# Kernel tuning notes

Measured on AMD Instinct MI355X. Metric: run time of the kernel, lower is better.

The kernel has to match this reference:

```python
import jax, jax.numpy as jnp
import numpy as np

K, S, P = 3, 2, 2  # kernel_size, stride, padding (dilation=1)


def _unfold(xp, k, s, oh, ow):
    """Extract k*k strided patches from a padded array.

    xp: (..., Hp, Wp) -> (..., k*k, oh, ow), window-position ordering (kh, kw)
    matching torch.nn.Unfold (channel-major handled by caller).
    """
    return jnp.stack(
        [xp[..., i:i + s * (oh - 1) + 1:s, j:j + s * (ow - 1) + 1:s]
         for i in range(K) for j in range(K)],
        axis=-3,
    )


def setup_inputs() -> dict:
    key = jax.random.key(0)
    x = jax.random.normal(key, (8, 256, 128, 128), dtype=jnp.float32)
    return {"x": x}


def reference(x):
    b, c, h, w = x.shape
    oh = (h - K + 2 * P) // S + 1
    ow = (w - K + 2 * P) // S + 1

    # channel-wise L2 norm, computed BEFORE unfolding (padding contributes 0 either way)
    n = jnp.sqrt(jnp.sum(x * x, axis=1))            # (b, h, w)
    n_pad = jnp.pad(n, ((0, 0), (P, P), (P, P)))
    n_patch = _unfold(n_pad, K, S, oh, ow)          # (b, k*k, oh, ow)
    # weighting_fn = softmax over the k*k window positions (torch dim=1 of unfolded norm)
    wts = jax.nn.softmax(n_patch, axis=1)           # (b, k*k, oh, ow)

    x_pad = jnp.pad(x, ((0, 0), (0, 0), (P, P), (P, P)))
    x_patch = _unfold(x_pad, K, S, oh, ow)          # (b, c, k*k, oh, ow)

    # weighted sum over window positions
    return jnp.sum(wts[:, None] * x_patch, axis=2)  # (b, c, oh, ow)
```

## Files before the change

### kernel.cpp

```cpp
#include <hip/hip_runtime.h>
#include <math.h>

#define BATCH 8
#define CH    256
#define H     128
#define W     128
#define HW    (H * W)
#define OH    65
#define OW    65
#define NPIX  (OH * OW)
#define TPB   512
#define WAVES 8
#define CPW   (CH / WAVES)

__global__ __launch_bounds__(TPB, 6) void fused_kernel(const float* __restrict__ x,
                                                       float* __restrict__ out) {
    const int b    = blockIdx.x & 7;
    const int oh   = blockIdx.x >> 3;
    const int tid  = threadIdx.x;
    const int lane = tid & 63;
    const int wv   = tid >> 6;

    int  rowc[3];
    bool rv[3];
    #pragma unroll
    for (int r = 0; r < 3; ++r) {
        int ih = oh * 2 + r - 2;
        rv[r]   = (unsigned)ih < (unsigned)H;
        rowc[r] = ih < 0 ? 0 : (ih > H - 1 ? H - 1 : ih);
    }

    __shared__ float part[WAVES][3][W];
    __shared__ float nrm[3][W];
    __shared__ float wls[OH][9];

    const float2* xw2 = (const float2*)x + (size_t)(b * CH + wv * CPW) * (HW / 2);
    const int base0 = rowc[0] * (W / 2) + lane;
    const int base1 = rowc[1] * (W / 2) + lane;
    const int base2 = rowc[2] * (W / 2) + lane;

    float2 a0 = {0.f, 0.f}, a1 = {0.f, 0.f}, a2 = {0.f, 0.f};
    #pragma unroll 8
    for (int c = 0; c < CPW; ++c) {
        const size_t cb = (size_t)c * (HW / 2);
        float2 v0 = xw2[cb + base0];
        float2 v1 = xw2[cb + base1];
        float2 v2 = xw2[cb + base2];
        a0.x += v0.x * v0.x; a0.y += v0.y * v0.y;
        a1.x += v1.x * v1.x; a1.y += v1.y * v1.y;
        a2.x += v2.x * v2.x; a2.y += v2.y * v2.y;
    }
    *(float2*)&part[wv][0][2 * lane] = a0;
    *(float2*)&part[wv][1][2 * lane] = a1;
    *(float2*)&part[wv][2][2 * lane] = a2;
    __syncthreads();

    if (tid < 3 * W) {
        int r = tid >> 7, col = tid & (W - 1);
        float s = 0.f;
        #pragma unroll
        for (int w = 0; w < WAVES; ++w) s += part[w][r][col];
        nrm[r][col] = sqrtf(s);
    }
    __syncthreads();

    if (tid < OH) {
        const int ow  = tid;
        const int iw0 = ow * 2 - 2;
        float nv[9];
        bool  val[9];
        float m = 0.0f;
        #pragma unroll
        for (int kh = 0; kh < 3; ++kh) {
            bool vh = rv[kh];
            #pragma unroll
            for (int kw = 0; kw < 3; ++kw) {
                int iw = iw0 + kw;
                int k  = kh * 3 + kw;
                bool v = vh && ((unsigned)iw < (unsigned)W);
                val[k] = v;
                nv[k]  = v ? nrm[kh][iw] : 0.0f;
                m = fmaxf(m, nv[k]);
            }
        }
        float denom = 0.0f, wt[9];
        #pragma unroll
        for (int k = 0; k < 9; ++k) {
            float e = __expf(nv[k] - m);
            denom += e;
            wt[k] = val[k] ? e : 0.0f;
        }
        float inv = 1.0f / denom;
        #pragma unroll
        for (int k = 0; k < 9; ++k) wls[ow][k] = wt[k] * inv;
    }
    __syncthreads();

    const float wA0 = wls[lane][2], wA1 = wls[lane][5], wA2 = wls[lane][8];
    const float wB0 = wls[lane + 1][0], wC0 = wls[lane + 1][1];
    const float wB1 = wls[lane + 1][3], wC1 = wls[lane + 1][4];
    const float wB2 = wls[lane + 1][6], wC2 = wls[lane + 1][7];

    float* ob = out + (size_t)(b * CH + wv * CPW) * NPIX + (size_t)oh * OW;
    #pragma unroll 4
    for (int c = 0; c < CPW; ++c) {
        const size_t cb = (size_t)c * (HW / 2);
        float2 v0 = xw2[cb + base0];
        float2 v1 = xw2[cb + base1];
        float2 v2 = xw2[cb + base2];
        float S = wB0 * v0.x + wC0 * v0.y
                + wB1 * v1.x + wC1 * v1.y
                + wB2 * v2.x + wC2 * v2.y;
        float T = wA0 * v0.x + wA1 * v1.x + wA2 * v2.x;
        float Sp = __shfl_up(S, 1);
        float res = (lane == 0) ? T : T + Sp;
        ob[(size_t)c * NPIX + lane] = res;
        if (lane == 63) ob[(size_t)c * NPIX + 64] = S;
    }
}

extern "C" void kernel_launch(void* const* d_in, const int* in_sizes, int n_in,
                              void* d_out, int out_size, void* d_ws, size_t ws_size,
                              hipStream_t stream) {
    const float* x = (const float*)d_in[0];
    float* out = (float*)d_out;
    (void)d_ws; (void)ws_size;
    fused_kernel<<<BATCH * OH, TPB, 0, stream>>>(x, out);
}
```

Baseline: 232.2 us.

## Split norm into separate pass and compute two output rows per block

The fused kernel is split in two. A norm kernel streams x once and writes per-pixel channel L2 norms to the workspace. The pool kernel then reads those norms and processes two output rows per block, loading 5 input rows instead of 3 per row, so the overlapping input row is reused within the block. This removes the redundant norm pass over x in every block. In exchange it adds a second launch and a workspace round trip, and the pool kernel has fewer blocks.

```diff
diff --git a/kernel.cpp b/kernel.cpp
--- a/kernel.cpp
+++ b/kernel.cpp
@@ -9,113 +9,141 @@
 #define OH    65
 #define OW    65
 #define NPIX  (OH * OW)
-#define TPB   512
-#define WAVES 8
-#define CPW   (CH / WAVES)
 
-__global__ __launch_bounds__(TPB, 6) void fused_kernel(const float* __restrict__ x,
-                                                       float* __restrict__ out) {
+__global__ __launch_bounds__(256) void norm_kernel(const float4* __restrict__ x4,
+                                                   float* __restrict__ nrm) {
+    const int b    = blockIdx.x >> 6;
+    const int t    = blockIdx.x & 63;
+    const int lane = threadIdx.x & 63;
+    const int wv   = threadIdx.x >> 6;
+
+    const float4* p = x4 + (size_t)(b * CH + wv * 64) * (HW / 4) + t * 64 + lane;
+    float4 a = {0.f, 0.f, 0.f, 0.f};
+    #pragma unroll 8
+    for (int c = 0; c < 64; ++c) {
+        float4 v = p[(size_t)c * (HW / 4)];
+        a.x += v.x * v.x; a.y += v.y * v.y;
+        a.z += v.z * v.z; a.w += v.w * v.w;
+    }
+    __shared__ float part[4][256];
+    ((float4*)part[wv])[lane] = a;
+    __syncthreads();
+    float s = part[0][threadIdx.x] + part[1][threadIdx.x]
+            + part[2][threadIdx.x] + part[3][threadIdx.x];
+    nrm[(size_t)b * HW + t * 256 + threadIdx.x] = sqrtf(s);
+}
+
+#define OHT   33
+#define K2TPB 512
+#define CPW   32
+
+__global__ __launch_bounds__(K2TPB) void pool_kernel(const float* __restrict__ x,
+                                                     const float* __restrict__ nrm,
+                                                     float* __restrict__ out) {
     const int b    = blockIdx.x & 7;
-    const int oh   = blockIdx.x >> 3;
+    const int ohT  = blockIdx.x >> 3;
+    const int oh0  = ohT * 2;
+    const bool hasB = (oh0 + 1) < OH;
     const int tid  = threadIdx.x;
     const int lane = tid & 63;
     const int wv   = tid >> 6;
 
-    int  rowc[3];
-    bool rv[3];
+    int rowc[5];
     #pragma unroll
-    for (int r = 0; r < 3; ++r) {
-        int ih = oh * 2 + r - 2;
-        rv[r]   = (unsigned)ih < (unsigned)H;
+    for (int r = 0; r < 5; ++r) {
+        int ih = oh0 * 2 - 2 + r;
         rowc[r] = ih < 0 ? 0 : (ih > H - 1 ? H - 1 : ih);
     }
 
-    __shared__ float part[WAVES][3][W];
-    __shared__ float nrm[3][W];
-    __shared__ float wls[OH][9];
+    __shared__ float ns[5][W];
+    __shared__ float wls[2 * OH][9];
+
+    for (int id = tid; id < 5 * W; id += K2TPB) {
+        int r = id >> 7, col = id & (W - 1);
+        ns[r][col] = nrm[(size_t)b * HW + rowc[r] * W + col];
+    }
+    __syncthreads();
+
+    if (tid < 2 * OH) {
+        int ohl = tid >= OH ? 1 : 0;
+        int ow  = tid - ohl * OH;
+        int oh  = oh0 + ohl;
+        if (oh < OH) {
+            int iw0 = ow * 2 - 2;
+            float nv[9]; bool val[9]; float m = 0.0f;
+            #pragma unroll
+            for (int kh = 0; kh < 3; ++kh) {
+                int ih = oh * 2 + kh - 2;
+                bool vh = (unsigned)ih < (unsigned)H;
+                int rL = 2 * ohl + kh;
+                #pragma unroll
+                for (int kw = 0; kw < 3; ++kw) {
+                    int iw = iw0 + kw;
+                    int k  = kh * 3 + kw;
+                    bool v = vh && ((unsigned)iw < (unsigned)W);
+                    val[k] = v;
+                    nv[k]  = v ? ns[rL][iw] : 0.0f;
+                    m = fmaxf(m, nv[k]);
+                }
+            }
+            float denom = 0.0f, wt[9];
+            #pragma unroll
+            for (int k = 0; k < 9; ++k) {
+                float e = __expf(nv[k] - m);
+                denom += e;
+                wt[k] = val[k] ? e : 0.0f;
+            }
+            float inv = 1.0f / denom;
+            #pragma unroll
+            for (int k = 0; k < 9; ++k) wls[tid][k] = wt[k] * inv;
+        }
+    }
+    __syncthreads();
+
+    const float aA0 = wls[lane][2],     aA1 = wls[lane][5],     aA2 = wls[lane][8];
+    const float aB0 = wls[lane + 1][0], aC0 = wls[lane + 1][1];
+    const float aB1 = wls[lane + 1][3], aC1 = wls[lane + 1][4];
+    const float aB2 = wls[lane + 1][6], aC2 = wls[lane + 1][7];
+    const float bA0 = wls[OH + lane][2],     bA1 = wls[OH + lane][5],     bA2 = wls[OH + lane][8];
+    const float bB0 = wls[OH + lane + 1][0], bC0 = wls[OH + lane + 1][1];
+    const float bB1 = wls[OH + lane + 1][3], bC1 = wls[OH + lane + 1][4];
+    const float bB2 = wls[OH + lane + 1][6], bC2 = wls[OH + lane + 1][7];
 
     const float2* xw2 = (const float2*)x + (size_t)(b * CH + wv * CPW) * (HW / 2);
     const int base0 = rowc[0] * (W / 2) + lane;
     const int base1 = rowc[1] * (W / 2) + lane;
     const int base2 = rowc[2] * (W / 2) + lane;
+    const int base3 = rowc[3] * (W / 2) + lane;
+    const int base4 = rowc[4] * (W / 2) + lane;
 
-    float2 a0 = {0.f, 0.f}, a1 = {0.f, 0.f}, a2 = {0.f, 0.f};
-    #pragma unroll 8
-    for (int c = 0; c < CPW; ++c) {
-        const size_t cb = (size_t)c * (HW / 2);
-        float2 v0 = xw2[cb + base0];
-        float2 v1 = xw2[cb + base1];
-        float2 v2 = xw2[cb + base2];
-        a0.x += v0.x * v0.x; a0.y += v0.y * v0.y;
-        a1.x += v1.x * v1.x; a1.y += v1.y * v1.y;
-        a2.x += v2.x * v2.x; a2.y += v2.y * v2.y;
-    }
-    *(float2*)&part[wv][0][2 * lane] = a0;
-    *(float2*)&part[wv][1][2 * lane] = a1;
-    *(float2*)&part[wv][2][2 * lane] = a2;
-    __syncthreads();
-
-    if (tid < 3 * W) {
-        int r = tid >> 7, col = tid & (W - 1);
-        float s = 0.f;
-        #pragma unroll
-        for (int w = 0; w < WAVES; ++w) s += part[w][r][col];
-        nrm[r][col] = sqrtf(s);
-    }
-    __syncthreads();
-
-    if (tid < OH) {
-        const int ow  = tid;
-        const int iw0 = ow * 2 - 2;
-        float nv[9];
-        bool  val[9];
-        float m = 0.0f;
-        #pragma unroll
-        for (int kh = 0; kh < 3; ++kh) {
-            bool vh = rv[kh];
-            #pragma unroll
-            for (int kw = 0; kw < 3; ++kw) {
-                int iw = iw0 + kw;
-                int k  = kh * 3 + kw;
-                bool v = vh && ((unsigned)iw < (unsigned)W);
-                val[k] = v;
-                nv[k]  = v ? nrm[kh][iw] : 0.0f;
-                m = fmaxf(m, nv[k]);
-            }
-        }
-        float denom = 0.0f, wt[9];
-        #pragma unroll
-        for (int k = 0; k < 9; ++k) {
-            float e = __expf(nv[k] - m);
-            denom += e;
-            wt[k] = val[k] ? e : 0.0f;
-        }
-        float inv = 1.0f / denom;
-        #pragma unroll
-        for (int k = 0; k < 9; ++k) wls[ow][k] = wt[k] * inv;
-    }
-    __syncthreads();
-
-    const float wA0 = wls[lane][2], wA1 = wls[lane][5], wA2 = wls[lane][8];
-    const float wB0 = wls[lane + 1][0], wC0 = wls[lane + 1][1];
-    const float wB1 = wls[lane + 1][3], wC1 = wls[lane + 1][4];
-    const float wB2 = wls[lane + 1][6], wC2 = wls[lane + 1][7];
-
-    float* ob = out + (size_t)(b * CH + wv * CPW) * NPIX + (size_t)oh * OW;
+    float* ob = out + (size_t)(b * CH + wv * CPW) * NPIX + (size_t)oh0 * OW;
     #pragma unroll 4
     for (int c = 0; c < CPW; ++c) {
         const size_t cb = (size_t)c * (HW / 2);
         float2 v0 = xw2[cb + base0];
         float2 v1 = xw2[cb + base1];
         float2 v2 = xw2[cb + base2];
-        float S = wB0 * v0.x + wC0 * v0.y
-                + wB1 * v1.x + wC1 * v1.y
-                + wB2 * v2.x + wC2 * v2.y;
-        float T = wA0 * v0.x + wA1 * v1.x + wA2 * v2.x;
-        float Sp = __shfl_up(S, 1);
-        float res = (lane == 0) ? T : T + Sp;
-        ob[(size_t)c * NPIX + lane] = res;
-        if (lane == 63) ob[(size_t)c * NPIX + 64] = S;
+        float SA = aB0 * v0.x + aC0 * v0.y
+                 + aB1 * v1.x + aC1 * v1.y
+                 + aB2 * v2.x + aC2 * v2.y;
+        float TA = aA0 * v0.x + aA1 * v1.x + aA2 * v2.x;
+        float SpA = __shfl_up(SA, 1);
+        float resA = (lane == 0) ? TA : TA + SpA;
+        float* oc = ob + (size_t)c * NPIX;
+        oc[lane] = resA;
+        if (lane == 63) oc[64] = SA;
+        if (hasB) {
+            float2 v3 = xw2[cb + base3];
+            float2 v4 = xw2[cb + base4];
+            float SB = bB0 * v2.x + bC0 * v2.y
+                     + bB1 * v3.x + bC1 * v3.y
+                     + bB2 * v4.x + bC2 * v4.y;
+            float TB = bA0 * v2.x + bA1 * v3.x + bA2 * v4.x;
+            float SpB = __shfl_up(SB, 1);
+            float resB = (lane == 0) ? TB : TB + SpB;
+            oc[OW + lane] = resB;
+            if (lane == 63) oc[OW + 64] = SB;
+        }
     }
 }
 
@@ -123,7 +151,9 @@
                               void* d_out, int out_size, void* d_ws, size_t ws_size,
                               hipStream_t stream) {
     const float* x = (const float*)d_in[0];
-    float* out = (float*)d_out;
-    (void)d_ws; (void)ws_size;
-    fused_kernel<<<BATCH * OH, TPB, 0, stream>>>(x, out);
+    float* out  = (float*)d_out;
+    float* nbuf = (float*)d_ws;
+
+    norm_kernel<<<512, 256, 0, stream>>>((const float4*)x, nbuf);
+    pool_kernel<<<BATCH * OHT, K2TPB, 0, stream>>>(x, nbuf, out);
 }
```

New measurement: 224.1 us. -3.5%, faster.

## Split channel-norm into separate kernel and split pooling across channel groups

Applied to the files above, without the earlier changes.

Computes the per-pixel channel L2 norm in a dedicated kernel that reads each input element once and stores norms in workspace. The pooling kernel then loads precomputed norms instead of recomputing them from overlapping rows, and splits channels into two groups to double the grid size. This cuts the redundant input reads caused by overlapping windows. In exchange it adds a second launch and a small workspace round-trip.

```diff
diff --git a/kernel.cpp b/kernel.cpp
--- a/kernel.cpp
+++ b/kernel.cpp
@@ -9,77 +9,76 @@
 #define OH    65
 #define OW    65
 #define NPIX  (OH * OW)
-#define TPB   512
-#define WAVES 8
-#define CPW   (CH / WAVES)
 
-__global__ __launch_bounds__(TPB, 6) void fused_kernel(const float* __restrict__ x,
-                                                       float* __restrict__ out) {
-    const int b    = blockIdx.x & 7;
-    const int oh   = blockIdx.x >> 3;
+__global__ __launch_bounds__(256) void norm_kernel(const float4* __restrict__ x4,
+                                                   float* __restrict__ nrm) {
+    const int b    = blockIdx.x >> 6;
+    const int t    = blockIdx.x & 63;
+    const int lane = threadIdx.x & 63;
+    const int wv   = threadIdx.x >> 6;
+
+    const float4* p = x4 + (size_t)(b * CH + wv * 64) * (HW / 4) + t * 64 + lane;
+    float4 a = {0.f, 0.f, 0.f, 0.f};
+    #pragma unroll 8
+    for (int c = 0; c < 64; ++c) {
+        float4 v = p[(size_t)c * (HW / 4)];
+        a.x += v.x * v.x; a.y += v.y * v.y;
+        a.z += v.z * v.z; a.w += v.w * v.w;
+    }
+    __shared__ float part[4][256];
+    ((float4*)part[wv])[lane] = a;
+    __syncthreads();
+    float s = part[0][threadIdx.x] + part[1][threadIdx.x]
+            + part[2][threadIdx.x] + part[3][threadIdx.x];
+    nrm[(size_t)b * HW + t * 256 + threadIdx.x] = sqrtf(s);
+}
+
+#define K2TPB 256
+#define CPW   32
+#define CGC   128
+
+__global__ __launch_bounds__(K2TPB) void pool_kernel(const float* __restrict__ x,
+                                                     const float* __restrict__ nrm,
+                                                     float* __restrict__ out) {
+    const int b   = blockIdx.x & 7;
+    const int rem = blockIdx.x >> 3;
+    const int oh  = rem % OH;
+    const int cg  = rem / OH;
     const int tid  = threadIdx.x;
     const int lane = tid & 63;
     const int wv   = tid >> 6;
 
     int  rowc[3];
-    bool rv[3];
     #pragma unroll
     for (int r = 0; r < 3; ++r) {
         int ih = oh * 2 + r - 2;
-        rv[r]   = (unsigned)ih < (unsigned)H;
         rowc[r] = ih < 0 ? 0 : (ih > H - 1 ? H - 1 : ih);
     }
 
-    __shared__ float part[WAVES][3][W];
-    __shared__ float nrm[3][W];
+    __shared__ float ns[3][W];
     __shared__ float wls[OH][9];
 
-    const float2* xw2 = (const float2*)x + (size_t)(b * CH + wv * CPW) * (HW / 2);
-    const int base0 = rowc[0] * (W / 2) + lane;
-    const int base1 = rowc[1] * (W / 2) + lane;
-    const int base2 = rowc[2] * (W / 2) + lane;
-
-    float2 a0 = {0.f, 0.f}, a1 = {0.f, 0.f}, a2 = {0.f, 0.f};
-    #pragma unroll 8
-    for (int c = 0; c < CPW; ++c) {
-        const size_t cb = (size_t)c * (HW / 2);
-        float2 v0 = xw2[cb + base0];
-        float2 v1 = xw2[cb + base1];
-        float2 v2 = xw2[cb + base2];
-        a0.x += v0.x * v0.x; a0.y += v0.y * v0.y;
-        a1.x += v1.x * v1.x; a1.y += v1.y * v1.y;
-        a2.x += v2.x * v2.x; a2.y += v2.y * v2.y;
-    }
-    *(float2*)&part[wv][0][2 * lane] = a0;
-    *(float2*)&part[wv][1][2 * lane] = a1;
-    *(float2*)&part[wv][2][2 * lane] = a2;
-    __syncthreads();
-
-    if (tid < 3 * W) {
-        int r = tid >> 7, col = tid & (W - 1);
-        float s = 0.f;
-        #pragma unroll
-        for (int w = 0; w < WAVES; ++w) s += part[w][r][col];
-        nrm[r][col] = sqrtf(s);
+    for (int id = tid; id < 3 * W; id += K2TPB) {
+        int r = id >> 7, col = id & (W - 1);
+        ns[r][col] = nrm[(size_t)b * HW + rowc[r] * W + col];
     }
     __syncthreads();
 
     if (tid < OH) {
         const int ow  = tid;
         const int iw0 = ow * 2 - 2;
-        float nv[9];
-        bool  val[9];
-        float m = 0.0f;
+        float nv[9]; bool val[9]; float m = 0.0f;
         #pragma unroll
         for (int kh = 0; kh < 3; ++kh) {
-            bool vh = rv[kh];
+            int ih = oh * 2 + kh - 2;
+            bool vh = (unsigned)ih < (unsigned)H;
             #pragma unroll
             for (int kw = 0; kw < 3; ++kw) {
                 int iw = iw0 + kw;
                 int k  = kh * 3 + kw;
                 bool v = vh && ((unsigned)iw < (unsigned)W);
                 val[k] = v;
-                nv[k]  = v ? nrm[kh][iw] : 0.0f;
+                nv[k]  = v ? ns[kh][iw] : 0.0f;
                 m = fmaxf(m, nv[k]);
             }
         }
@@ -101,8 +100,15 @@
     const float wB1 = wls[lane + 1][3], wC1 = wls[lane + 1][4];
     const float wB2 = wls[lane + 1][6], wC2 = wls[lane + 1][7];
 
-    float* ob = out + (size_t)(b * CH + wv * CPW) * NPIX + (size_t)oh * OW;
-    #pragma unroll 4
+    const float2* xw2 = (const float2*)x
+        + (size_t)(b * CH + cg * CGC + wv * CPW) * (HW / 2);
+    const int base0 = rowc[0] * (W / 2) + lane;
+    const int base1 = rowc[1] * (W / 2) + lane;
+    const int base2 = rowc[2] * (W / 2) + lane;
+
+    float* ob = out + (size_t)(b * CH + cg * CGC + wv * CPW) * NPIX
+                    + (size_t)oh * OW;
+    #pragma unroll 8
     for (int c = 0; c < CPW; ++c) {
         const size_t cb = (size_t)c * (HW / 2);
         float2 v0 = xw2[cb + base0];
@@ -114,8 +120,9 @@
         float T = wA0 * v0.x + wA1 * v1.x + wA2 * v2.x;
         float Sp = __shfl_up(S, 1);
         float res = (lane == 0) ? T : T + Sp;
-        ob[(size_t)c * NPIX + lane] = res;
-        if (lane == 63) ob[(size_t)c * NPIX + 64] = S;
+        float* oc = ob + (size_t)c * NPIX;
+        oc[lane] = res;
+        if (lane == 63) oc[64] = S;
     }
 }
 
@@ -123,7 +130,9 @@
                               void* d_out, int out_size, void* d_ws, size_t ws_size,
                               hipStream_t stream) {
     const float* x = (const float*)d_in[0];
-    float* out = (float*)d_out;
-    (void)d_ws; (void)ws_size;
-    fused_kernel<<<BATCH * OH, TPB, 0, stream>>>(x, out);
+    float* out  = (float*)d_out;
+    float* nbuf = (float*)d_ws;
+
+    norm_kernel<<<512, 256, 0, stream>>>((const float4*)x, nbuf);
+    pool_kernel<<<BATCH * OH * 2, K2TPB, 0, stream>>>(x, nbuf, out);
 }
```

Result: faster. 218.6 us (-5.8%).
